# Kernel optimization log

Measured on AMD Instinct MI355X. Metric: run time of the kernel, lower is better.

The kernel has to match this reference:

```python
import jax, jax.numpy as jnp
import numpy as np


def _sparsify24(w):
    """2:4 structured sparsity: per contiguous group of 4 along the last dim,
    keep the 2 largest-magnitude entries, zero the other 2 (soft_threshold24)."""
    m, n = w.shape
    g = w.reshape(m, n // 4, 4)
    a = jnp.abs(g)
    # 2nd-largest magnitude in each group = index 2 of ascending sort of 4
    thresh = jnp.sort(a, axis=-1)[..., 2:3]
    mask = a >= thresh
    return (g * mask).reshape(m, n)


def setup_inputs() -> dict:
    key = jax.random.key(0)
    k1, k2, k3 = jax.random.split(key, 3)
    B, S, DIN, DOUT = 4, 4096, 1024, 1024
    x = jax.random.normal(k1, (B, S, DIN), dtype=jnp.float32)
    weight = jax.random.normal(k2, (DIN, DOUT), dtype=jnp.float32) * 0.02
    bias = jax.random.normal(k3, (DOUT,), dtype=jnp.float32) * 0.02
    sparse_scale = jnp.ones((1,), dtype=jnp.float32)
    return {"x": x, "weight": weight, "bias": bias, "sparse_scale": sparse_scale}


def reference(x, weight, bias, sparse_scale):
    # get_sparse_weight: cast weight to fp16, apply 2:4 sparsity, multiply by
    # learnable fp32 scale (promotes to fp32 as in torch half*float).
    w_sparse = _sparsify24(weight.astype(jnp.float16)).astype(jnp.float32) * sparse_scale
    # fake_fp8_mm: both operands cast to fp16, accumulate/output in fp32.
    a = x.reshape(-1, x.shape[-1]).astype(jnp.float16)          # [B*S, DIN]
    b = w_sparse.astype(jnp.float16)                             # [DIN, DOUT]
    out = jnp.matmul(a, b, preferred_element_type=jnp.float32)   # [B*S, DOUT] fp32
    out = out.reshape(*x.shape[:-1], -1) + bias
    return out
```

## Files before the change

kernel.cpp:

```cpp
#include <hip/hip_runtime.h>
#include <hip/hip_fp16.h>
#include <stdint.h>

#define M_TOT 16384
#define N_TOT 1024
#define K_TOT 1024

typedef _Float16 f16x8 __attribute__((ext_vector_type(8)));
typedef float f32x4 __attribute__((ext_vector_type(4)));

__device__ inline void gl2lds16(const void* g, void* l) {
    __builtin_amdgcn_global_load_lds(
        (const __attribute__((address_space(1))) void*)(uintptr_t)(g),
        (__attribute__((address_space(3))) void*)(uint32_t)(uintptr_t)(l),
        16, 0, 0);
}

__global__ void prep_weight(const float* __restrict__ W,
                            const float* __restrict__ scale_p,
                            _Float16* __restrict__ wT) {
    const float scale = scale_p[0];
    int idx = blockIdx.x * blockDim.x + threadIdx.x;
    int k = idx & (K_TOT - 1);
    int g = idx >> 10;
    float4 w4 = *(const float4*)&W[(size_t)k * N_TOT + g * 4];
    _Float16 h0 = (_Float16)w4.x, h1 = (_Float16)w4.y, h2 = (_Float16)w4.z, h3 = (_Float16)w4.w;
    float a0 = fabsf((float)h0), a1 = fabsf((float)h1), a2 = fabsf((float)h2), a3 = fabsf((float)h3);
    float lo01 = fminf(a0, a1), hi01 = fmaxf(a0, a1);
    float lo23 = fminf(a2, a3), hi23 = fmaxf(a2, a3);
    float s2 = fmaxf(fminf(hi01, hi23), fmaxf(lo01, lo23));
    float v0 = (a0 >= s2) ? (float)h0 : 0.0f;
    float v1 = (a1 >= s2) ? (float)h1 : 0.0f;
    float v2 = (a2 >= s2) ? (float)h2 : 0.0f;
    float v3 = (a3 >= s2) ? (float)h3 : 0.0f;
    size_t nb = (size_t)(g * 4) * K_TOT + k;
    wT[nb + 0 * K_TOT] = (_Float16)(v0 * scale);
    wT[nb + 1 * K_TOT] = (_Float16)(v1 * scale);
    wT[nb + 2 * K_TOT] = (_Float16)(v2 * scale);
    wT[nb + 3 * K_TOT] = (_Float16)(v3 * scale);
}

__global__ void cast_x(const float* __restrict__ X, _Float16* __restrict__ Xh) {
    size_t i = ((size_t)blockIdx.x * blockDim.x + threadIdx.x) * 8;
    float4 x0 = *(const float4*)&X[i];
    float4 x1 = *(const float4*)&X[i + 4];
    f16x8 h;
    h[0] = (_Float16)x0.x; h[1] = (_Float16)x0.y; h[2] = (_Float16)x0.z; h[3] = (_Float16)x0.w;
    h[4] = (_Float16)x1.x; h[5] = (_Float16)x1.y; h[6] = (_Float16)x1.z; h[7] = (_Float16)x1.w;
    *(f16x8*)&Xh[i] = h;
}

__global__ void __launch_bounds__(256) gemm_bt(const _Float16* __restrict__ A,
                                               const _Float16* __restrict__ Bt,
                                               const float* __restrict__ bias,
                                               float* __restrict__ C) {
    __shared__ _Float16 sA[128 * 32];
    __shared__ _Float16 sB[128 * 32];
    const int tid = threadIdx.x;
    const int id = blockIdx.x;
    const int by = id & 127;
    const int bx = id >> 7;
    const int wave = tid >> 6;
    const int lane = tid & 63;
    const int wm = wave >> 1, wn = wave & 1;
    const int quad = lane >> 4;
    const int l16 = lane & 15;

    const int srow = tid >> 2;
    const int scol = (tid & 3) * 8;

    const _Float16* gA = A + ((size_t)(by * 128 + srow)) * K_TOT + scol;
    const _Float16* gB = Bt + ((size_t)(bx * 128 + srow)) * K_TOT + scol;
    _Float16* lA = sA + srow * 32 + scol;
    _Float16* lB = sB + srow * 32 + scol;

    f32x4 acc[4][4];
#pragma unroll
    for (int i = 0; i < 4; ++i)
#pragma unroll
        for (int j = 0; j < 4; ++j)
            acc[i][j] = (f32x4){0.f, 0.f, 0.f, 0.f};

    for (int k0 = 0; k0 < K_TOT; k0 += 32) {
        __syncthreads();
        gl2lds16(gA + k0, lA);
        gl2lds16(gA + k0 + (size_t)64 * K_TOT, lA + 64 * 32);
        gl2lds16(gB + k0, lB);
        gl2lds16(gB + k0 + (size_t)64 * K_TOT, lB + 64 * 32);
        __syncthreads();

        f16x8 af[4], bf[4];
#pragma unroll
        for (int i = 0; i < 4; ++i) {
            af[i] = *(const f16x8*)&sA[(wm * 64 + i * 16 + l16) * 32 + quad * 8];
            bf[i] = *(const f16x8*)&sB[(wn * 64 + i * 16 + l16) * 32 + quad * 8];
        }
#pragma unroll
        for (int i = 0; i < 4; ++i)
#pragma unroll
            for (int j = 0; j < 4; ++j)
                acc[i][j] = __builtin_amdgcn_mfma_f32_16x16x32_f16(af[i], bf[j], acc[i][j], 0, 0, 0);
    }

#pragma unroll
    for (int j = 0; j < 4; ++j) {
        const int col = bx * 128 + wn * 64 + j * 16 + l16;
        const float bj = bias[col];
#pragma unroll
        for (int i = 0; i < 4; ++i) {
            const int row0 = by * 128 + wm * 64 + i * 16 + quad * 4;
#pragma unroll
            for (int r = 0; r < 4; ++r) {
                __builtin_nontemporal_store(acc[i][j][r] + bj,
                                            &C[(size_t)(row0 + r) * N_TOT + col]);
            }
        }
    }
}

extern "C" void kernel_launch(void* const* d_in, const int* in_sizes, int n_in,
                              void* d_out, int out_size, void* d_ws, size_t ws_size,
                              hipStream_t stream) {
    const float* x      = (const float*)d_in[0];
    const float* weight = (const float*)d_in[1];
    const float* bias   = (const float*)d_in[2];
    const float* sscale = (const float*)d_in[3];
    float* out = (float*)d_out;

    _Float16* wT = (_Float16*)d_ws;
    _Float16* xh = (_Float16*)((char*)d_ws + (size_t)2 * 1024 * 1024);

    prep_weight<<<(K_TOT * N_TOT / 4) / 256, 256, 0, stream>>>(weight, sscale, wT);
    cast_x<<<(M_TOT * K_TOT / 8) / 256, 256, 0, stream>>>(x, xh);
    gemm_bt<<<1024, 256, 0, stream>>>(xh, wT, bias, out);
}
```

Baseline: 179.4 us.

## Tile weight transpose through LDS, double K-step per sync in GEMM, plain stores

The weight prep kernel now transposes 64x64 tiles through shared memory so writes to the transposed fp16 weight are coalesced instead of strided. The GEMM loads two 32-wide K slabs per barrier pair, halving the number of __syncthreads per K sweep at the cost of doubled LDS use. The output stores switch from nontemporal to ordinary stores. These are several unrelated tweaks bundled together.

After: 160.3 us. -10.6%, faster.

```diff
diff --git a/kernel.cpp b/kernel.cpp
--- a/kernel.cpp
+++ b/kernel.cpp
@@ -8,6 +8,7 @@
 
 typedef _Float16 f16x8 __attribute__((ext_vector_type(8)));
 typedef float f32x4 __attribute__((ext_vector_type(4)));
+typedef unsigned short ushort4v __attribute__((ext_vector_type(4)));
 
 __device__ inline void gl2lds16(const void* g, void* l) {
     __builtin_amdgcn_global_load_lds(
@@ -16,28 +17,37 @@
         16, 0, 0);
 }
 
-__global__ void prep_weight(const float* __restrict__ W,
-                            const float* __restrict__ scale_p,
-                            _Float16* __restrict__ wT) {
+__global__ void __launch_bounds__(256) prep_weight(const float* __restrict__ W,
+                                                   const float* __restrict__ scale_p,
+                                                   _Float16* __restrict__ wT) {
+    __shared__ _Float16 sT[64 * 68 + 4];
     const float scale = scale_p[0];
-    int idx = blockIdx.x * blockDim.x + threadIdx.x;
-    int k = idx & (K_TOT - 1);
-    int g = idx >> 10;
-    float4 w4 = *(const float4*)&W[(size_t)k * N_TOT + g * 4];
-    _Float16 h0 = (_Float16)w4.x, h1 = (_Float16)w4.y, h2 = (_Float16)w4.z, h3 = (_Float16)w4.w;
-    float a0 = fabsf((float)h0), a1 = fabsf((float)h1), a2 = fabsf((float)h2), a3 = fabsf((float)h3);
-    float lo01 = fminf(a0, a1), hi01 = fmaxf(a0, a1);
-    float lo23 = fminf(a2, a3), hi23 = fmaxf(a2, a3);
-    float s2 = fmaxf(fminf(hi01, hi23), fmaxf(lo01, lo23));
-    float v0 = (a0 >= s2) ? (float)h0 : 0.0f;
-    float v1 = (a1 >= s2) ? (float)h1 : 0.0f;
-    float v2 = (a2 >= s2) ? (float)h2 : 0.0f;
-    float v3 = (a3 >= s2) ? (float)h3 : 0.0f;
-    size_t nb = (size_t)(g * 4) * K_TOT + k;
-    wT[nb + 0 * K_TOT] = (_Float16)(v0 * scale);
-    wT[nb + 1 * K_TOT] = (_Float16)(v1 * scale);
-    wT[nb + 2 * K_TOT] = (_Float16)(v2 * scale);
-    wT[nb + 3 * K_TOT] = (_Float16)(v3 * scale);
+    const int k0 = (blockIdx.x & 15) * 64;
+    const int n0 = (blockIdx.x >> 4) * 64;
+    const int tid = threadIdx.x;
+    const int r = tid >> 4;
+    const int c4 = (tid & 15) * 4;
+#pragma unroll
+    for (int p = 0; p < 4; ++p) {
+        const int k = p * 16 + r;
+        float4 w4 = *(const float4*)&W[(size_t)(k0 + k) * N_TOT + n0 + c4];
+        _Float16 h0 = (_Float16)w4.x, h1 = (_Float16)w4.y, h2 = (_Float16)w4.z, h3 = (_Float16)w4.w;
+        float a0 = fabsf((float)h0), a1 = fabsf((float)h1), a2 = fabsf((float)h2), a3 = fabsf((float)h3);
+        float lo01 = fminf(a0, a1), hi01 = fmaxf(a0, a1);
+        float lo23 = fminf(a2, a3), hi23 = fmaxf(a2, a3);
+        float s2 = fmaxf(fminf(hi01, hi23), fmaxf(lo01, lo23));
+        sT[(c4 + 0) * 68 + k] = (_Float16)(((a0 >= s2) ? (float)h0 : 0.0f) * scale);
+        sT[(c4 + 1) * 68 + k] = (_Float16)(((a1 >= s2) ? (float)h1 : 0.0f) * scale);
+        sT[(c4 + 2) * 68 + k] = (_Float16)(((a2 >= s2) ? (float)h2 : 0.0f) * scale);
+        sT[(c4 + 3) * 68 + k] = (_Float16)(((a3 >= s2) ? (float)h3 : 0.0f) * scale);
+    }
+    __syncthreads();
+#pragma unroll
+    for (int p = 0; p < 4; ++p) {
+        const int n = p * 16 + r;
+        ushort4v v = *(const ushort4v*)&sT[n * 68 + c4];
+        *(ushort4v*)&wT[(size_t)(n0 + n) * K_TOT + k0 + c4] = v;
+    }
 }
 
 __global__ void cast_x(const float* __restrict__ X, _Float16* __restrict__ Xh) {
@@ -54,8 +64,8 @@
                                                const _Float16* __restrict__ Bt,
                                                const float* __restrict__ bias,
                                                float* __restrict__ C) {
-    __shared__ _Float16 sA[128 * 32];
-    __shared__ _Float16 sB[128 * 32];
+    __shared__ _Float16 sA[2][128 * 32];
+    __shared__ _Float16 sB[2][128 * 32];
     const int tid = threadIdx.x;
     const int id = blockIdx.x;
     const int by = id & 127;
@@ -71,8 +81,7 @@
 
     const _Float16* gA = A + ((size_t)(by * 128 + srow)) * K_TOT + scol;
     const _Float16* gB = Bt + ((size_t)(bx * 128 + srow)) * K_TOT + scol;
-    _Float16* lA = sA + srow * 32 + scol;
-    _Float16* lB = sB + srow * 32 + scol;
+    const int soff = srow * 32 + scol;
 
     f32x4 acc[4][4];
 #pragma unroll
@@ -81,25 +90,32 @@
         for (int j = 0; j < 4; ++j)
             acc[i][j] = (f32x4){0.f, 0.f, 0.f, 0.f};
 
-    for (int k0 = 0; k0 < K_TOT; k0 += 32) {
+    for (int k0 = 0; k0 < K_TOT; k0 += 64) {
         __syncthreads();
-        gl2lds16(gA + k0, lA);
-        gl2lds16(gA + k0 + (size_t)64 * K_TOT, lA + 64 * 32);
-        gl2lds16(gB + k0, lB);
-        gl2lds16(gB + k0 + (size_t)64 * K_TOT, lB + 64 * 32);
+        gl2lds16(gA + k0,                         &sA[0][soff]);
+        gl2lds16(gA + k0 + (size_t)64 * K_TOT,    &sA[0][soff + 64 * 32]);
+        gl2lds16(gA + k0 + 32,                    &sA[1][soff]);
+        gl2lds16(gA + k0 + 32 + (size_t)64 * K_TOT, &sA[1][soff + 64 * 32]);
+        gl2lds16(gB + k0,                         &sB[0][soff]);
+        gl2lds16(gB + k0 + (size_t)64 * K_TOT,    &sB[0][soff + 64 * 32]);
+        gl2lds16(gB + k0 + 32,                    &sB[1][soff]);
+        gl2lds16(gB + k0 + 32 + (size_t)64 * K_TOT, &sB[1][soff + 64 * 32]);
         __syncthreads();
 
-        f16x8 af[4], bf[4];
 #pragma unroll
-        for (int i = 0; i < 4; ++i) {
-            af[i] = *(const f16x8*)&sA[(wm * 64 + i * 16 + l16) * 32 + quad * 8];
-            bf[i] = *(const f16x8*)&sB[(wn * 64 + i * 16 + l16) * 32 + quad * 8];
+        for (int s = 0; s < 2; ++s) {
+            f16x8 af[4], bf[4];
+#pragma unroll
+            for (int i = 0; i < 4; ++i) {
+                af[i] = *(const f16x8*)&sA[s][(wm * 64 + i * 16 + l16) * 32 + quad * 8];
+                bf[i] = *(const f16x8*)&sB[s][(wn * 64 + i * 16 + l16) * 32 + quad * 8];
+            }
+#pragma unroll
+            for (int i = 0; i < 4; ++i)
+#pragma unroll
+                for (int j = 0; j < 4; ++j)
+                    acc[i][j] = __builtin_amdgcn_mfma_f32_16x16x32_f16(af[i], bf[j], acc[i][j], 0, 0, 0);
         }
-#pragma unroll
-        for (int i = 0; i < 4; ++i)
-#pragma unroll
-            for (int j = 0; j < 4; ++j)
-                acc[i][j] = __builtin_amdgcn_mfma_f32_16x16x32_f16(af[i], bf[j], acc[i][j], 0, 0, 0);
     }
 
 #pragma unroll
@@ -111,8 +127,7 @@
             const int row0 = by * 128 + wm * 64 + i * 16 + quad * 4;
 #pragma unroll
             for (int r = 0; r < 4; ++r) {
-                __builtin_nontemporal_store(acc[i][j][r] + bj,
-                                            &C[(size_t)(row0 + r) * N_TOT + col]);
+                C[(size_t)(row0 + r) * N_TOT + col] = acc[i][j][r] + bj;
             }
         }
     }
@@ -130,7 +145,7 @@
     _Float16* wT = (_Float16*)d_ws;
     _Float16* xh = (_Float16*)((char*)d_ws + (size_t)2 * 1024 * 1024);
 
-    prep_weight<<<(K_TOT * N_TOT / 4) / 256, 256, 0, stream>>>(weight, sscale, wT);
+    prep_weight<<<256, 256, 0, stream>>>(weight, sscale, wT);
     cast_x<<<(M_TOT * K_TOT / 8) / 256, 256, 0, stream>>>(x, xh);
     gemm_bt<<<1024, 256, 0, stream>>>(xh, wT, bias, out);
 }
```
